# Kernel optimization log

Hardware: AMD Instinct MI355X
Metric: run time of the kernel (lower is better)

Reference implementation:

```python
import jax, jax.numpy as jnp
import numpy as np

INVALID_TOKEN_ID = -1
B, K, V = 128, 8, 128000  # batch, spec length, vocab


def setup_inputs() -> dict:
    key = jax.random.key(0)
    k1, k2 = jax.random.split(key)
    draft_token_ids = jax.random.randint(k1, (B, K), 0, V, dtype=jnp.int64 if jax.config.jax_enable_x64 else jnp.int32)
    # target probs over vocab for B*(K+1) sampled positions
    target_probs = jax.random.uniform(k2, (B * (K + 1), V), dtype=jnp.float32)
    return {"draft_token_ids": draft_token_ids, "target_probs": target_probs}


def reference(draft_token_ids, target_probs):
    b, k = draft_token_ids.shape
    # greedy target tokens: argmax over vocab, reshaped to [B, K+1]
    output_token_ids = jnp.argmax(target_probs, axis=-1).reshape(b, k + 1).astype(draft_token_ids.dtype)
    # accept draft tokens while they match target greedy tokens (prefix match)
    accept_mask = jnp.cumprod((output_token_ids[:, :-1] == draft_token_ids).astype(jnp.int32), axis=1)
    valid_mask = output_token_ids != INVALID_TOKEN_ID
    generate_mask = jnp.concatenate(
        [accept_mask.astype(bool), jnp.zeros((b, 1), dtype=bool)], axis=1
    ) & valid_mask
    # first rejected position also emits the (bonus/corrected) target token
    zeros_mask = ~generate_mask
    first_zero_idx = jnp.argmax(zeros_mask.astype(jnp.float32), axis=1)
    rows_with_zero = jnp.any(zeros_mask, axis=1)
    fix = (jnp.arange(k + 1)[None, :] == first_zero_idx[:, None]) & rows_with_zero[:, None]
    generate_mask = generate_mask | fix
    return jnp.where(generate_mask, output_token_ids, INVALID_TOKEN_ID)
```

## Files before the change

kernel.cpp:

```cpp
#include <hip/hip_runtime.h>
#include <math.h>

#define INVALID_TOKEN_ID (-1)
constexpr int BB = 128;
constexpr int KK = 8;
constexpr int VV = 128000;
constexpr int ROWS = BB * (KK + 1);
constexpr int THREADS = 256;

__global__ __launch_bounds__(THREADS) void argmax_rows_kernel(
    const float* __restrict__ probs, int* __restrict__ amax_out) {
    const int row = blockIdx.x;
    const int tid = threadIdx.x;
    const float4* __restrict__ p4 =
        (const float4*)(probs + (size_t)row * VV);

    float best = -INFINITY;
    int bestIdx = VV;

    #pragma unroll 5
    for (int i = tid; i < VV / 4; i += THREADS) {
        float4 v = p4[i];
        int base = i * 4;
        if (v.x > best) { best = v.x; bestIdx = base; }
        if (v.y > best) { best = v.y; bestIdx = base + 1; }
        if (v.z > best) { best = v.z; bestIdx = base + 2; }
        if (v.w > best) { best = v.w; bestIdx = base + 3; }
    }

    #pragma unroll
    for (int off = 32; off > 0; off >>= 1) {
        float ov = __shfl_down(best, off, 64);
        int   oi = __shfl_down(bestIdx, off, 64);
        if (ov > best || (ov == best && oi < bestIdx)) {
            best = ov;
            bestIdx = oi;
        }
    }

    __shared__ float s_v[THREADS / 64];
    __shared__ int   s_i[THREADS / 64];
    const int wave = tid >> 6;
    const int lane = tid & 63;
    if (lane == 0) {
        s_v[wave] = best;
        s_i[wave] = bestIdx;
    }
    __syncthreads();
    if (tid == 0) {
        #pragma unroll
        for (int w = 1; w < THREADS / 64; ++w) {
            if (s_v[w] > best || (s_v[w] == best && s_i[w] < bestIdx)) {
                best = s_v[w];
                bestIdx = s_i[w];
            }
        }
        amax_out[row] = bestIdx;
    }
}

__global__ __launch_bounds__(128) void finalize_kernel(
    const int* __restrict__ draft, const int* __restrict__ amax,
    int* __restrict__ out) {
    const int b = threadIdx.x;
    if (b >= BB) return;
    const int* arow = amax + b * (KK + 1);
    const int* drow = draft + b * KK;
    int r = 0;
    while (r < KK && arow[r] == drow[r]) ++r;
    int* orow = out + b * (KK + 1);
    #pragma unroll
    for (int j = 0; j <= KK; ++j) {
        orow[j] = (j <= r) ? arow[j] : INVALID_TOKEN_ID;
    }
}

extern "C" void kernel_launch(void* const* d_in, const int* in_sizes, int n_in,
                              void* d_out, int out_size, void* d_ws, size_t ws_size,
                              hipStream_t stream) {
    const int*   draft = (const int*)d_in[0];
    const float* probs = (const float*)d_in[1];
    int* out  = (int*)d_out;
    int* amax = (int*)d_ws;

    argmax_rows_kernel<<<ROWS, THREADS, 0, stream>>>(probs, amax);
    finalize_kernel<<<1, 128, 0, stream>>>(draft, amax, out);
}
```

Baseline: 749.1 us.

## Split argmax rows across blocks with packed 64-bit value-index reduction

Each vocabulary row is split into five segments processed by separate blocks, raising block count for better bandwidth utilization, with register double-buffered batched loads. Partial results are packed as float bits with inverted index into 64-bit keys so reductions are single comparisons, and the finalize kernel merges the partials. The packing assumes non-negative probabilities.

Result: faster. 732.8 us (-2.2%).

```diff
diff --git a/kernel.cpp b/kernel.cpp
--- a/kernel.cpp
+++ b/kernel.cpp
@@ -8,71 +8,112 @@
 constexpr int ROWS = BB * (KK + 1);
 constexpr int THREADS = 256;
 
-__global__ __launch_bounds__(THREADS) void argmax_rows_kernel(
-    const float* __restrict__ probs, int* __restrict__ amax_out) {
-    const int row = blockIdx.x;
+constexpr int SPLIT   = 5;
+constexpr int NPART   = ROWS * SPLIT;
+constexpr int CHUNK4  = (VV / 4) / SPLIT;
+constexpr int ITERS   = CHUNK4 / THREADS;
+constexpr int BATCH   = 5;
+constexpr int NBATCH  = ITERS / BATCH;
+
+typedef float f32x4 __attribute__((ext_vector_type(4)));
+
+__device__ __forceinline__ unsigned long long pack_vi(float v, int idx) {
+    return ((unsigned long long)__float_as_uint(v) << 32) |
+           (unsigned int)(~idx);
+}
+
+__global__ __launch_bounds__(THREADS) void argmax_part_kernel(
+    const float* __restrict__ probs, unsigned long long* __restrict__ part) {
+    const int bid = blockIdx.x;
+    const int row = bid / SPLIT;
+    const int seg = bid % SPLIT;
     const int tid = threadIdx.x;
-    const float4* __restrict__ p4 =
-        (const float4*)(probs + (size_t)row * VV);
 
-    float best = -INFINITY;
-    int bestIdx = VV;
+    const f32x4* __restrict__ p4 =
+        (const f32x4*)(probs + (size_t)row * VV) + seg * CHUNK4;
 
-    #pragma unroll 5
-    for (int i = tid; i < VV / 4; i += THREADS) {
-        float4 v = p4[i];
-        int base = i * 4;
-        if (v.x > best) { best = v.x; bestIdx = base; }
-        if (v.y > best) { best = v.y; bestIdx = base + 1; }
-        if (v.z > best) { best = v.z; bestIdx = base + 2; }
-        if (v.w > best) { best = v.w; bestIdx = base + 3; }
+    float best = -1.0f;
+    int bestIdx = 0;
+
+    f32x4 cur[BATCH], nxt[BATCH];
+
+    #pragma unroll
+    for (int u = 0; u < BATCH; ++u)
+        cur[u] = p4[tid + u * THREADS];
+
+    #pragma unroll
+    for (int g = 0; g < NBATCH; ++g) {
+        if (g + 1 < NBATCH) {
+            #pragma unroll
+            for (int u = 0; u < BATCH; ++u)
+                nxt[u] = p4[tid + ((g + 1) * BATCH + u) * THREADS];
+        }
+        #pragma unroll
+        for (int u = 0; u < BATCH; ++u) {
+            f32x4 v = cur[u];
+            float m = fmaxf(fmaxf(v[0], v[1]), fmaxf(v[2], v[3]));
+            if (m > best) {
+                int q    = tid + (g * BATCH + u) * THREADS;
+                int base = (seg * CHUNK4 + q) * 4;
+                best = m;
+                bestIdx = (v[0] == m) ? base
+                        : (v[1] == m) ? base + 1
+                        : (v[2] == m) ? base + 2
+                        :               base + 3;
+            }
+        }
+        if (g + 1 < NBATCH) {
+            #pragma unroll
+            for (int u = 0; u < BATCH; ++u) cur[u] = nxt[u];
+        }
     }
+
+    unsigned long long packed = pack_vi(best, bestIdx);
 
     #pragma unroll
     for (int off = 32; off > 0; off >>= 1) {
-        float ov = __shfl_down(best, off, 64);
-        int   oi = __shfl_down(bestIdx, off, 64);
-        if (ov > best || (ov == best && oi < bestIdx)) {
-            best = ov;
-            bestIdx = oi;
-        }
+        unsigned long long o = __shfl_down(packed, off, 64);
+        packed = (o > packed) ? o : packed;
     }
 
-    __shared__ float s_v[THREADS / 64];
-    __shared__ int   s_i[THREADS / 64];
+    __shared__ unsigned long long s_p[THREADS / 64];
     const int wave = tid >> 6;
     const int lane = tid & 63;
-    if (lane == 0) {
-        s_v[wave] = best;
-        s_i[wave] = bestIdx;
-    }
+    if (lane == 0) s_p[wave] = packed;
     __syncthreads();
     if (tid == 0) {
         #pragma unroll
-        for (int w = 1; w < THREADS / 64; ++w) {
-            if (s_v[w] > best || (s_v[w] == best && s_i[w] < bestIdx)) {
-                best = s_v[w];
-                bestIdx = s_i[w];
-            }
-        }
-        amax_out[row] = bestIdx;
+        for (int w = 1; w < THREADS / 64; ++w)
+            packed = (s_p[w] > packed) ? s_p[w] : packed;
+        part[bid] = packed;
     }
 }
 
-__global__ __launch_bounds__(128) void finalize_kernel(
-    const int* __restrict__ draft, const int* __restrict__ amax,
-    int* __restrict__ out) {
+__global__ __launch_bounds__(128) void reduce_finalize_kernel(
+    const unsigned long long* __restrict__ part,
+    const int* __restrict__ draft, int* __restrict__ out) {
     const int b = threadIdx.x;
     if (b >= BB) return;
-    const int* arow = amax + b * (KK + 1);
+
+    int toks[KK + 1];
+    #pragma unroll
+    for (int j = 0; j <= KK; ++j) {
+        const unsigned long long* pr = part + (size_t)(b * (KK + 1) + j) * SPLIT;
+        unsigned long long m = pr[0];
+        #pragma unroll
+        for (int s = 1; s < SPLIT; ++s)
+            m = (pr[s] > m) ? pr[s] : m;
+        toks[j] = (int)(~(unsigned int)(m & 0xFFFFFFFFull));
+    }
+
     const int* drow = draft + b * KK;
     int r = 0;
-    while (r < KK && arow[r] == drow[r]) ++r;
+    while (r < KK && toks[r] == drow[r]) ++r;
+
     int* orow = out + b * (KK + 1);
     #pragma unroll
-    for (int j = 0; j <= KK; ++j) {
-        orow[j] = (j <= r) ? arow[j] : INVALID_TOKEN_ID;
-    }
+    for (int j = 0; j <= KK; ++j)
+        orow[j] = (j <= r) ? toks[j] : INVALID_TOKEN_ID;
 }
 
 extern "C" void kernel_launch(void* const* d_in, const int* in_sizes, int n_in,
@@ -80,9 +121,9 @@
                               hipStream_t stream) {
     const int*   draft = (const int*)d_in[0];
     const float* probs = (const float*)d_in[1];
-    int* out  = (int*)d_out;
-    int* amax = (int*)d_ws;
+    int* out = (int*)d_out;
+    unsigned long long* part = (unsigned long long*)d_ws;
 
-    argmax_rows_kernel<<<ROWS, THREADS, 0, stream>>>(probs, amax);
-    finalize_kernel<<<1, 128, 0, stream>>>(draft, amax, out);
+    argmax_part_kernel<<<NPART, THREADS, 0, stream>>>(probs, part);
+    reduce_finalize_kernel<<<1, 128, 0, stream>>>(part, draft, out);
 }
```
